# Performance work log

Hardware: AMD Instinct MI355X
Metric: run time of the kernel (lower is better)

The kernel has to match this reference:

```python
import jax, jax.numpy as jnp
import numpy as np

B, H, W, C = 32, 56, 56, 512
WS, SHIFT, NH = 7, 3, 16
N = WS * WS
NW = (H // WS) * (W // WS)
HID = 4 * C
EPS = 1e-5


def _np_constants():
    # log-spaced relative coords table (SwinV2 CPB input), pretrained_window_size=[0,0]
    rh = np.arange(-(WS - 1), WS, dtype=np.float32)
    tbl = np.stack(np.meshgrid(rh, rh, indexing='ij'), axis=-1)  # (2*WS-1, 2*WS-1, 2)
    tbl = tbl / (WS - 1) * 8.0
    tbl = np.sign(tbl) * np.log2(np.abs(tbl) + 1.0) / np.log2(8.0)
    coords = np.stack(np.meshgrid(np.arange(WS), np.arange(WS), indexing='ij'))
    cf = coords.reshape(2, -1)
    rc = (cf[:, :, None] - cf[:, None, :]).transpose(1, 2, 0).copy()  # (N,N,2)
    rc[..., 0] += WS - 1
    rc[..., 1] += WS - 1
    rc[..., 0] *= 2 * WS - 1
    rpi = rc.sum(-1)  # (N,N) indices into the (2*WS-1)^2 table
    # shifted-window attention mask
    img = np.zeros((H, W), dtype=np.float32)
    sl = (slice(0, -WS), slice(-WS, -SHIFT), slice(-SHIFT, None))
    cnt = 0
    for hs in sl:
        for ws in sl:
            img[hs, ws] = cnt
            cnt += 1
    mw = img.reshape(H // WS, WS, W // WS, WS).transpose(0, 2, 1, 3).reshape(-1, N)
    am = mw[:, None, :] - mw[:, :, None]
    attn_mask = np.where(am != 0, -100.0, 0.0).astype(np.float32)  # (NW,N,N)
    return tbl.reshape(-1, 2).astype(np.float32), rpi.reshape(-1), attn_mask

TBL_NP, RPI_NP, MASK_NP = _np_constants()


def _ln(x, g, b):
    mu = jnp.mean(x, -1, keepdims=True)
    var = jnp.mean((x - mu) ** 2, -1, keepdims=True)
    return (x - mu) * jax.lax.rsqrt(var + EPS) * g + b


def _win_part(x):  # (B,H,W,C) -> (B*NW, N, C)
    x = x.reshape(B, H // WS, WS, W // WS, WS, C).transpose(0, 1, 3, 2, 4, 5)
    return x.reshape(-1, N, C)


def _win_rev(w):  # (B*NW, N, C) -> (B,H,W,C)
    x = w.reshape(B, H // WS, W // WS, WS, WS, C).transpose(0, 1, 3, 2, 4, 5)
    return x.reshape(B, H, W, C)


def setup_inputs() -> dict:
    key = jax.random.key(0)
    ks = jax.random.split(key, 8)
    s = 0.02
    return {
        'x': jax.random.normal(ks[0], (B, H * W, C), jnp.float32),
        'qkv_w': jax.random.normal(ks[1], (3 * C, C), jnp.float32) * s,
        'q_bias': jnp.zeros((C,), jnp.float32),
        'v_bias': jnp.zeros((C,), jnp.float32),
        'logit_scale': jnp.log(10.0) * jnp.ones((NH, 1, 1), jnp.float32),
        'cpb_w1': jax.random.normal(ks[2], (512, 2), jnp.float32) * s,
        'cpb_b1': jnp.zeros((512,), jnp.float32),
        'cpb_w2': jax.random.normal(ks[3], (NH, 512), jnp.float32) * s,
        'proj_w': jax.random.normal(ks[4], (C, C), jnp.float32) * s,
        'proj_b': jnp.zeros((C,), jnp.float32),
        'norm1_g': jnp.ones((C,), jnp.float32),
        'norm1_b': jnp.zeros((C,), jnp.float32),
        'fc1_w': jax.random.normal(ks[5], (HID, C), jnp.float32) * s,
        'fc1_b': jnp.zeros((HID,), jnp.float32),
        'fc2_w': jax.random.normal(ks[6], (C, HID), jnp.float32) * s,
        'fc2_b': jnp.zeros((C,), jnp.float32),
        'norm2_g': jnp.ones((C,), jnp.float32),
        'norm2_b': jnp.zeros((C,), jnp.float32),
    }


def reference(x, qkv_w, q_bias, v_bias, logit_scale, cpb_w1, cpb_b1, cpb_w2,
              proj_w, proj_b, norm1_g, norm1_b, fc1_w, fc1_b, fc2_w, fc2_b,
              norm2_g, norm2_b):
    tbl = jnp.asarray(TBL_NP)
    mask = jnp.asarray(MASK_NP)
    shortcut = x
    xi = x.reshape(B, H, W, C)
    xi = jnp.roll(xi, shift=(-SHIFT, -SHIFT), axis=(1, 2))
    xw = _win_part(xi)  # (B*NW, N, C)
    qkv_bias = jnp.concatenate([q_bias, jnp.zeros_like(v_bias), v_bias])
    qkv = xw @ qkv_w.T + qkv_bias
    qkv = qkv.reshape(-1, N, 3, NH, C // NH).transpose(2, 0, 3, 1, 4)
    q, k, v = qkv[0], qkv[1], qkv[2]  # (B_, NH, N, hd)
    qn = q / jnp.maximum(jnp.linalg.norm(q, axis=-1, keepdims=True), 1e-12)
    kn = k / jnp.maximum(jnp.linalg.norm(k, axis=-1, keepdims=True), 1e-12)
    scale = jnp.exp(jnp.minimum(logit_scale, jnp.log(100.0)))  # (NH,1,1)
    attn = jnp.einsum('bhnd,bhmd->bhnm', qn, kn) * scale
    # CPB MLP -> relative position bias
    hcb = jax.nn.relu(tbl @ cpb_w1.T + cpb_b1)       # (169, 512)
    bias_tbl = hcb @ cpb_w2.T                        # (169, NH)
    rpb = bias_tbl[RPI_NP].reshape(N, N, NH).transpose(2, 0, 1)
    rpb = 16.0 * jax.nn.sigmoid(rpb)
    attn = attn + rpb[None]
    attn = attn.reshape(B, NW, NH, N, N) + mask[None, :, None]
    attn = jax.nn.softmax(attn.reshape(-1, NH, N, N), axis=-1)
    out = jnp.einsum('bhnm,bhmd->bhnd', attn, v).transpose(0, 2, 1, 3).reshape(-1, N, C)
    out = out @ proj_w.T + proj_b
    xi = _win_rev(out)
    xi = jnp.roll(xi, shift=(SHIFT, SHIFT), axis=(1, 2)).reshape(B, H * W, C)
    x = shortcut + _ln(xi, norm1_g, norm1_b)  # SwinV2 post-norm residual
    hmlp = jax.nn.gelu(x @ fc1_w.T + fc1_b, approximate=False)
    m = hmlp @ fc2_w.T + fc2_b
    x = x + _ln(m, norm2_g, norm2_b)
    return x
```

## Files before the change

### kernel.cpp

```cpp
#include <hip/hip_runtime.h>

typedef unsigned short u16;
typedef unsigned int   u32;

using f32x4  = __attribute__((ext_vector_type(4))) float;
using bf16x8 = __attribute__((ext_vector_type(8))) short;

__device__ __forceinline__ float bf2f(u16 u){
  union { u32 i; float f; } x; x.i = ((u32)u) << 16; return x.f;
}
__device__ __forceinline__ u16 f2bf(float f){
  union { float f; u32 i; } x; x.f = f;
  u32 r = x.i + 0x7FFFu + ((x.i >> 16) & 1u);
  return (u16)(r >> 16);
}
__device__ __forceinline__ float gelu_f(float v){
  float u = 0.7978845608f * v * (1.f + 0.044715f*v*v);
  float e = __expf(2.f*u);
  return 0.5f*v*(2.f - 2.f/(e + 1.f));
}

__device__ __forceinline__ void glds16(const void* g, void* l){
  __builtin_amdgcn_global_load_lds(
      (const __attribute__((address_space(1))) unsigned int*)g,
      (__attribute__((address_space(3))) unsigned int*)(unsigned int)(unsigned long long)l,
      16, 0, 0);
}

__device__ __forceinline__ int rollmap(int m){
  int win = m / 49, n = m % 49;
  int b  = win >> 6, wi = win & 63;
  int wh = wi >> 3, ww = wi & 7;
  int r = n / 7, c = n % 7;
  int sh = wh*7 + r + 3; if (sh >= 56) sh -= 56;
  int sw = ww*7 + c + 3; if (sw >= 56) sw -= 56;
  return b*3136 + sh*56 + sw;
}

template<int EPI, int AMODE, int NT>
__global__ __launch_bounds__(256) void gemm_bt(const u16* __restrict__ A,
      const u16* __restrict__ Bw, const float* __restrict__ bias,
      void* __restrict__ outp, int M, int N, int nbn)
{
  constexpr int K = NT * 32;
  __shared__ __align__(16) char LDS[3*16384];
  const int t    = threadIdx.x;
  const int lane = t & 63, wave = t >> 6;
  const int wm = wave >> 1, wn = wave & 1;

  const int gl = ((blockIdx.x & 7) * ((int)gridDim.x >> 3)) + (blockIdx.x >> 3);
  const int bm = gl / nbn, bn = gl - bm*nbn;

  const int r0 = t >> 2;
  const int sc = t & 3;
  const int dc = sc ^ ((r0 >> 1) & 3);

  const u16* gB0 = Bw + (size_t)(bn*128 + r0)*K + dc*8;
  const u16* gB1 = gB0 + (size_t)64*K;
  const u16* gA0; const u16* gA1;
  if constexpr (AMODE == 0){
    gA0 = A + (size_t)(bm*128 + r0)*K + dc*8;
    gA1 = gA0 + (size_t)64*K;
  } else {
    gA0 = A + (size_t)rollmap(bm*128 + r0     )*K + dc*8;
    gA1 = A + (size_t)rollmap(bm*128 + r0 + 64)*K + dc*8;
  }

  const int lr = lane & 15, lk = lane >> 4;
  int offA[4], offB[4];
#pragma unroll
  for (int i = 0; i < 4; ++i){
    int ar = wm*64 + i*16 + lr;
    offA[i] = ar*64 + ((lk ^ ((ar >> 1) & 3)) * 16);
    int br = wn*64 + i*16 + lr;
    offB[i] = br*64 + ((lk ^ ((br >> 1) & 3)) * 16);
  }

  f32x4 acc[4][4];
#pragma unroll
  for (int i = 0; i < 4; ++i)
#pragma unroll
    for (int j = 0; j < 4; ++j) acc[i][j] = (f32x4){0.f, 0.f, 0.f, 0.f};

  auto STAGE = [&](int kt, int buf){
    char* Ld = LDS + buf*16384;
    glds16(gA0 + kt, Ld +         wave*1024);
    glds16(gA1 + kt, Ld +  4096 + wave*1024);
    glds16(gB0 + kt, Ld +  8192 + wave*1024);
    glds16(gB1 + kt, Ld + 12288 + wave*1024);
  };
  auto COMPUTE = [&](int buf){
    const char* Ld = LDS + buf*16384;
    bf16x8 fa[4], fb[4];
#pragma unroll
    for (int i = 0; i < 4; ++i){
      fa[i] = *(const bf16x8*)(Ld + offA[i]);
      fb[i] = *(const bf16x8*)(Ld + 8192 + offB[i]);
    }
#pragma unroll
    for (int i = 0; i < 4; ++i)
#pragma unroll
      for (int j = 0; j < 4; ++j)
        acc[i][j] = __builtin_amdgcn_mfma_f32_16x16x32_bf16(fa[i], fb[j], acc[i][j], 0, 0, 0);
  };

  STAGE(0, 0);
  STAGE(32, 1);
  asm volatile("s_waitcnt vmcnt(4)" ::: "memory");
  __builtin_amdgcn_s_barrier();
  asm volatile("" ::: "memory");

  if constexpr (NT <= 24){
#pragma unroll
    for (int t2 = 0; t2 < NT; ++t2){
      if (t2 + 2 < NT) STAGE((t2 + 2) * 32, (t2 + 2) % 3);
      COMPUTE(t2 % 3);
      if (t2 + 2 < NT){
        asm volatile("s_waitcnt vmcnt(4) lgkmcnt(0)" ::: "memory");
      } else if (t2 + 1 < NT){
        asm volatile("s_waitcnt vmcnt(0) lgkmcnt(0)" ::: "memory");
      }
      if (t2 + 1 < NT){
        __builtin_amdgcn_s_barrier();
        asm volatile("" ::: "memory");
      }
    }
  } else {
    int cur = 0;
    for (int t2 = 0; t2 + 2 < NT; ++t2){
      int nx2 = cur + 2; if (nx2 >= 3) nx2 -= 3;
      STAGE((t2 + 2) * 32, nx2);
      COMPUTE(cur);
      asm volatile("s_waitcnt vmcnt(4) lgkmcnt(0)" ::: "memory");
      __builtin_amdgcn_s_barrier();
      asm volatile("" ::: "memory");
      ++cur; if (cur == 3) cur = 0;
    }
    COMPUTE(cur);
    asm volatile("s_waitcnt vmcnt(0) lgkmcnt(0)" ::: "memory");
    __builtin_amdgcn_s_barrier();
    asm volatile("" ::: "memory");
    ++cur; if (cur == 3) cur = 0;
    COMPUTE(cur);
  }

#pragma unroll
  for (int i = 0; i < 4; ++i){
#pragma unroll
    for (int j = 0; j < 4; ++j){
      int cm = bm*128 + wm*64 + i*16 + (lane >> 4)*4;
      int cn = bn*128 + wn*64 + j*16 + (lane & 15);
      float bv = bias[cn];
#pragma unroll
      for (int r = 0; r < 4; ++r){
        float v = acc[i][j][r] + bv;
        if (EPI == 2) v = gelu_f(v);
        if (EPI == 1) ((float*)outp)[(size_t)(cm + r)*N + cn] = v;
        else          ((u16*)  outp)[(size_t)(cm + r)*N + cn] = f2bf(v);
      }
    }
  }
}

__global__ __launch_bounds__(256, 2) void attn_mfma(const u16* __restrict__ qkv,
      const float* __restrict__ rpb, const float* __restrict__ ls,
      u16* __restrict__ outp)
{
  __shared__ __align__(16) u16 Pl[4][64*72];
  __shared__ __align__(16) u16 Vl[4][32*72];
  __shared__ unsigned char regid[64];
  const int tid  = threadIdx.x, lane = tid & 63, wave = tid >> 6;
  const int lc = lane & 15, lg = lane >> 4;
  const int pair = blockIdx.x*4 + wave;
  const int win = pair >> 4, h = pair & 15;

  const u16* qb = qkv + (size_t)win*49*1536 + h*32;
  const u16* kb = qb + 512;
  const u16* vb = qb + 1024;

  if (tid < 49){
    int wi = win & 63, wh = wi >> 3, ww = wi & 7;
    int q7 = (tid*37) >> 8, r7 = tid - q7*7;
    int gh = wh*7 + q7, gw = ww*7 + r7;
    int rh = gh < 49 ? 0 : (gh < 53 ? 1 : 2);
    int rw = gw < 49 ? 0 : (gw < 53 ? 1 : 2);
    regid[tid] = (unsigned char)(rh*3 + rw);
  }

  u16* V = &Vl[wave][0];
#pragma unroll
  for (int it = 0; it < 4; ++it){
    int ch = it*64 + lane;
    int n = ch >> 2, oct = ch & 3;
    union { int4 i4; u16 s[8]; } v8;
    if (n < 49) v8.i4 = *(const int4*)(vb + (size_t)n*1536 + oct*8);
    else        v8.i4 = make_int4(0,0,0,0);
#pragma unroll
    for (int q = 0; q < 8; ++q) V[(oct*8 + q)*72 + n] = v8.s[q];
  }

  const float scale = __expf(fminf(ls[h], 4.6051702f));
  bf16x8 qf[4], kf[4];
#pragma unroll
  for (int ti = 0; ti < 4; ++ti){
    const int n = ti*16 + lc;
    {
      union { int4 i4; u16 s[8]; } raw;
      raw.i4 = *(const int4*)(qb + (size_t)n*1536 + lg*8);
      float f[8]; float ss = 0.f;
#pragma unroll
      for (int q = 0; q < 8; ++q){ f[q] = bf2f(raw.s[q]); ss += f[q]*f[q]; }
      ss += __shfl_xor(ss, 16); ss += __shfl_xor(ss, 32);
      const float inv = scale / fmaxf(sqrtf(ss), 1e-12f);
      union { short s[8]; bf16x8 v; } o;
#pragma unroll
      for (int q = 0; q < 8; ++q) o.s[q] = (short)f2bf(f[q]*inv);
      qf[ti] = o.v;
    }
    {
      union { int4 i4; u16 s[8]; } raw;
      raw.i4 = *(const int4*)(kb + (size_t)n*1536 + lg*8);
      float f[8]; float ss = 0.f;
#pragma unroll
      for (int q = 0; q < 8; ++q){ f[q] = bf2f(raw.s[q]); ss += f[q]*f[q]; }
      ss += __shfl_xor(ss, 16); ss += __shfl_xor(ss, 32);
      const float inv = 1.f / fmaxf(sqrtf(ss), 1e-12f);
      union { short s[8]; bf16x8 v; } o;
#pragma unroll
      for (int q = 0; q < 8; ++q) o.s[q] = (short)f2bf(f[q]*inv);
      kf[ti] = o.v;
    }
  }
  __syncthreads();

  f32x4 acc[4][4];
#pragma unroll
  for (int i = 0; i < 4; ++i)
#pragma unroll
    for (int j = 0; j < 4; ++j) acc[i][j] = (f32x4){0.f,0.f,0.f,0.f};
#pragma unroll
  for (int i = 0; i < 4; ++i)
#pragma unroll
    for (int j = 0; j < 4; ++j)
      acc[i][j] = __builtin_amdgcn_mfma_f32_16x16x32_bf16(qf[i], kf[j], acc[i][j], 0, 0, 0);

  u16* P = &Pl[wave][0];
  int rj[4];
#pragma unroll
  for (int tj = 0; tj < 4; ++tj){
    int j = tj*16 + lc;
    rj[tj] = (int)regid[j < 49 ? j : 0];
  }
  const float* rpbh = rpb + h*2401;
#pragma unroll
  for (int ti = 0; ti < 4; ++ti){
#pragma unroll
    for (int r = 0; r < 4; ++r){
      const int i = ti*16 + lg*4 + r;
      const bool iv = i < 49;
      const int ic = iv ? i : 0;
      const int ri = (int)regid[ic];
      const float* rrow = rpbh + ic*49;
      float sv[4];
#pragma unroll
      for (int tj = 0; tj < 4; ++tj){
        const int j = tj*16 + lc;
        float t2 = acc[ti][tj][r] + rrow[j < 49 ? j : 0];
        if (ri != rj[tj]) t2 -= 100.f;
        sv[tj] = (iv && j < 49) ? t2 : -1e30f;
      }
      float mx = fmaxf(fmaxf(sv[0],sv[1]), fmaxf(sv[2],sv[3]));
      mx = fmaxf(mx, __shfl_xor(mx, 1));
      mx = fmaxf(mx, __shfl_xor(mx, 2));
      mx = fmaxf(mx, __shfl_xor(mx, 4));
      mx = fmaxf(mx, __shfl_xor(mx, 8));
      float p[4], sum = 0.f;
#pragma unroll
      for (int tj = 0; tj < 4; ++tj){ p[tj] = __expf(sv[tj] - mx); sum += p[tj]; }
      sum += __shfl_xor(sum, 1); sum += __shfl_xor(sum, 2);
      sum += __shfl_xor(sum, 4); sum += __shfl_xor(sum, 8);
      const float rs = __builtin_amdgcn_rcpf(sum);
#pragma unroll
      for (int tj = 0; tj < 4; ++tj) P[i*72 + tj*16 + lc] = f2bf(p[tj]*rs);
    }
  }
  __syncthreads();

  f32x4 o[4][2];
#pragma unroll
  for (int i = 0; i < 4; ++i){ o[i][0] = (f32x4){0.f,0.f,0.f,0.f}; o[i][1] = (f32x4){0.f,0.f,0.f,0.f}; }
#pragma unroll
  for (int ks = 0; ks < 2; ++ks){
    bf16x8 pa[4], vf[2];
#pragma unroll
    for (int ti = 0; ti < 4; ++ti)
      pa[ti] = *(const bf16x8*)((const char*)P + (ti*16 + lc)*144 + (ks*4 + lg)*16);
#pragma unroll
    for (int tc = 0; tc < 2; ++tc)
      vf[tc] = *(const bf16x8*)((const char*)V + (tc*16 + lc)*144 + (ks*4 + lg)*16);
#pragma unroll
    for (int ti = 0; ti < 4; ++ti)
#pragma unroll
      for (int tc = 0; tc < 2; ++tc)
        o[ti][tc] = __builtin_amdgcn_mfma_f32_16x16x32_bf16(pa[ti], vf[tc], o[ti][tc], 0, 0, 0);
  }

#pragma unroll
  for (int ti = 0; ti < 4; ++ti){
#pragma unroll
    for (int tc = 0; tc < 2; ++tc){
#pragma unroll
      for (int r = 0; r < 4; ++r){
        const int i = ti*16 + lg*4 + r;
        if (i < 49)
          outp[((size_t)win*49 + i)*512 + h*32 + tc*16 + lc] = f2bf(o[ti][tc][r]);
      }
    }
  }
}

__global__ __launch_bounds__(256) void ln1_kernel(const u16* __restrict__ xb,
      const u16* __restrict__ y, const float* __restrict__ g, const float* __restrict__ bt,
      float* __restrict__ xout, u16* __restrict__ xbf)
{
  __shared__ float red[8];
  const int t = blockIdx.x;
  const int b = t / 3136, s = t % 3136;
  const int hh = s / 56, ww2 = s % 56;
  int ph = hh + 53; if (ph >= 56) ph -= 56;
  int pw = ww2 + 53; if (pw >= 56) pw -= 56;
  const int win = b*64 + (ph/7)*8 + (pw/7);
  const int n   = (ph%7)*7 + (pw%7);
  const u16* yr = y + ((size_t)win*49 + n)*512;
  const int c = threadIdx.x * 2;
  u32 u = *(const u32*)(yr + c);
  float vx = bf2f((u16)(u & 0xffff)), vy = bf2f((u16)(u >> 16));
  float sum = vx + vy, sq = vx*vx + vy*vy;
#pragma unroll
  for (int off = 32; off; off >>= 1){ sum += __shfl_xor(sum, off); sq += __shfl_xor(sq, off); }
  if ((threadIdx.x & 63) == 0){ red[threadIdx.x >> 6] = sum; red[(threadIdx.x >> 6) + 4] = sq; }
  __syncthreads();
  sum = red[0]+red[1]+red[2]+red[3];
  sq  = red[4]+red[5]+red[6]+red[7];
  const float mu  = sum * (1.f/512.f);
  const float inv = rsqrtf(fmaxf(sq * (1.f/512.f) - mu*mu, 0.f) + 1e-5f);
  u32 ux = *(const u32*)(xb + (size_t)t*512 + c);
  float o0 = bf2f((u16)(ux & 0xffff)) + (vx - mu)*inv*g[c]   + bt[c];
  float o1 = bf2f((u16)(ux >> 16))    + (vy - mu)*inv*g[c+1] + bt[c+1];
  float* orow = xout + (size_t)t*512;
  orow[c] = o0; orow[c+1] = o1;
  *(u32*)(xbf + (size_t)t*512 + c) = (u32)f2bf(o0) | ((u32)f2bf(o1) << 16);
}

__global__ __launch_bounds__(256) void ln2_kernel(const u16* __restrict__ m,
      const float* __restrict__ g, const float* __restrict__ bt, float* __restrict__ out)
{
  __shared__ float red[8];
  const int t = blockIdx.x;
  const int c = threadIdx.x * 2;
  u32 u = *(const u32*)(m + (size_t)t*512 + c);
  float v0 = bf2f((u16)(u & 0xffff)), v1 = bf2f((u16)(u >> 16));
  float sum = v0 + v1, sq = v0*v0 + v1*v1;
#pragma unroll
  for (int off = 32; off; off >>= 1){ sum += __shfl_xor(sum, off); sq += __shfl_xor(sq, off); }
  if ((threadIdx.x & 63) == 0){ red[threadIdx.x >> 6] = sum; red[(threadIdx.x >> 6) + 4] = sq; }
  __syncthreads();
  sum = red[0]+red[1]+red[2]+red[3];
  sq  = red[4]+red[5]+red[6]+red[7];
  const float mu  = sum * (1.f/512.f);
  const float inv = rsqrtf(fmaxf(sq * (1.f/512.f) - mu*mu, 0.f) + 1e-5f);
  float* orow = out + (size_t)t*512;
  orow[c]   += (v0 - mu)*inv*g[c]   + bt[c];
  orow[c+1] += (v1 - mu)*inv*g[c+1] + bt[c+1];
}

__global__ void cast_bf16_kernel(const float* __restrict__ in, u16* __restrict__ out, int n4){
  int i = blockIdx.x*256 + threadIdx.x;
  if (i >= n4) return;
  float4 v = *(const float4*)(in + (size_t)i*4);
  u32 lo = (u32)f2bf(v.x) | ((u32)f2bf(v.y) << 16);
  u32 hi = (u32)f2bf(v.z) | ((u32)f2bf(v.w) << 16);
  *(uint2*)(out + (size_t)i*4) = make_uint2(lo, hi);
}
__global__ void qkvbias_kernel(const float* __restrict__ qb, const float* __restrict__ vb,
                               float* __restrict__ out){
  int i = blockIdx.x*256 + threadIdx.x;
  if (i >= 1536) return;
  out[i] = i < 512 ? qb[i] : (i < 1024 ? 0.f : vb[i - 1024]);
}
__device__ __forceinline__ float cpb_coord(int d){
  float v = (float)(d - 6) * (8.f/6.f);
  float m = log2f(fabsf(v) + 1.f) * (1.f/3.f);
  return v > 0.f ? m : (v < 0.f ? -m : 0.f);
}
__global__ void cpb_kernel(const float* __restrict__ w1, const float* __restrict__ b1,
                           const float* __restrict__ w2, float* __restrict__ btbl){
  int idx = blockIdx.x*256 + threadIdx.x;
  if (idx >= 169*16) return;
  int e = idx >> 4, h = idx & 15;
  float t0 = cpb_coord(e / 13), t1 = cpb_coord(e % 13);
  float acc = 0.f;
  for (int jj = 0; jj < 512; ++jj){
    float hid = fmaxf(t0*w1[jj*2] + t1*w1[jj*2+1] + b1[jj], 0.f);
    acc += hid * w2[h*512 + jj];
  }
  btbl[e*16 + h] = acc;
}
__global__ void rpb_kernel(const float* __restrict__ btbl, float* __restrict__ rpb){
  int idx = blockIdx.x*256 + threadIdx.x;
  if (idx >= 16*49*49) return;
  int hh = idx / 2401, ij = idx % 2401, i = ij / 49, j = ij % 49;
  int dr = i/7 - j/7 + 6, dc = i%7 - j%7 + 6;
  float bb = btbl[(dr*13 + dc)*16 + hh];
  rpb[idx] = 16.f / (1.f + __expf(-bb));
}

extern "C" void kernel_launch(void* const* d_in, const int* in_sizes, int n_in,
                              void* d_out, int out_size, void* d_ws, size_t ws_size,
                              hipStream_t stream)
{
  const float* x    = (const float*)d_in[0];
  const float* qkvw = (const float*)d_in[1];
  const float* qb   = (const float*)d_in[2];
  const float* vb   = (const float*)d_in[3];
  const float* ls   = (const float*)d_in[4];
  const float* cw1  = (const float*)d_in[5];
  const float* cb1  = (const float*)d_in[6];
  const float* cw2  = (const float*)d_in[7];
  const float* pw   = (const float*)d_in[8];
  const float* pb   = (const float*)d_in[9];
  const float* n1g  = (const float*)d_in[10];
  const float* n1b  = (const float*)d_in[11];
  const float* f1w  = (const float*)d_in[12];
  const float* f1b  = (const float*)d_in[13];
  const float* f2w  = (const float*)d_in[14];
  const float* f2b  = (const float*)d_in[15];
  const float* n2g  = (const float*)d_in[16];
  const float* n2b  = (const float*)d_in[17];

  char* ws = (char*)d_ws;
  const size_t SZ_BIG = (size_t)100352 * 2048 * 2;
  const size_t SZ_MID = (size_t)100352 * 512  * 2;
  size_t o = SZ_BIG + SZ_MID;
  u16* wqkv  = (u16*)(ws + o); o += (size_t)1536*512*2;
  u16* wproj = (u16*)(ws + o); o += (size_t)512*512*2;
  u16* wfc1  = (u16*)(ws + o); o += (size_t)2048*512*2;
  u16* wfc2  = (u16*)(ws + o); o += (size_t)512*2048*2;
  float* qkvbias = (float*)(ws + o); o += 1536*4;
  float* btbl    = (float*)(ws + o); o += 2704*4;
  float* rpb     = (float*)(ws + o); o += 38416*4;

  u16*   xbf   = (u16*)ws;
  u16*   qkvo  = (u16*)(ws + (size_t)100352*512*2);
  u16*   y_h   = qkvo;
  u16*   big_h = (u16*)ws;
  u16*   mid   = (u16*)(ws + SZ_BIG);
  float* out   = (float*)d_out;

  cast_bf16_kernel<<<768,  256, 0, stream>>>(qkvw, wqkv, 1536*512/4);
  cast_bf16_kernel<<<256,  256, 0, stream>>>(pw,  wproj, 512*512/4);
  cast_bf16_kernel<<<1024, 256, 0, stream>>>(f1w, wfc1, 2048*512/4);
  cast_bf16_kernel<<<1024, 256, 0, stream>>>(f2w, wfc2, 512*2048/4);
  qkvbias_kernel<<<6, 256, 0, stream>>>(qb, vb, qkvbias);
  cpb_kernel<<<11, 256, 0, stream>>>(cw1, cb1, cw2, btbl);
  rpb_kernel<<<151, 256, 0, stream>>>(btbl, rpb);
  cast_bf16_kernel<<<50176, 256, 0, stream>>>(x, xbf, 100352*512/4);

  gemm_bt<0,2,16><<<784*12, 256, 0, stream>>>(xbf, wqkv, qkvbias,
                                              (void*)qkvo, 100352, 1536, 12);
  attn_mfma<<<8192, 256, 0, stream>>>(qkvo, rpb, ls, mid);
  gemm_bt<0,0,16><<<784*4, 256, 0, stream>>>(mid, wproj, pb,
                                             (void*)y_h, 100352, 512, 4);
  ln1_kernel<<<100352, 256, 0, stream>>>(xbf, y_h, n1g, n1b, out, mid);
  gemm_bt<2,0,16><<<784*16, 256, 0, stream>>>(mid, wfc1, f1b,
                                              (void*)big_h, 100352, 2048, 16);
  gemm_bt<0,0,64><<<784*4, 256, 0, stream>>>(big_h, wfc2, f2b,
                                             (void*)mid, 100352, 512, 4);
  ln2_kernel<<<100352, 256, 0, stream>>>(mid, n2g, n2b, out);
}
```

Baseline: 1.559 ms.

## Rewrite GEMM as 256x256 tile, 8-wave kernel with ping-pong staged loads

Replaces the 128x128, 4-wave GEMM with a 256x256 tile, 8-wave kernel. It uses 64-wide K steps, two 64KB LDS buffers and a new XOR swizzle. Loads for the next tiles are interleaved between four MFMA sub-phases, with barriers and s_setprio raising MFMA priority. The goal is more data reuse per byte loaded and better overlap of global-to-LDS traffic with compute for all four dense GEMMs. In exchange it uses 128KB of LDS per block, more accumulator registers and many more barriers, which could limit occupancy.

```diff
diff --git a/kernel.cpp b/kernel.cpp
--- a/kernel.cpp
+++ b/kernel.cpp
@@ -37,126 +37,169 @@
   return b*3136 + sh*56 + sw;
 }
 
-template<int EPI, int AMODE, int NT>
-__global__ __launch_bounds__(256) void gemm_bt(const u16* __restrict__ A,
+template<int EPI, int AMODE, int NKT>
+__global__ __launch_bounds__(512, 2) void gemm_bt(const u16* __restrict__ A,
       const u16* __restrict__ Bw, const float* __restrict__ bias,
       void* __restrict__ outp, int M, int N, int nbn)
 {
-  constexpr int K = NT * 32;
-  __shared__ __align__(16) char LDS[3*16384];
+  constexpr int K = NKT * 64;
+  __shared__ __align__(16) char LDS[2*65536];
   const int t    = threadIdx.x;
   const int lane = t & 63, wave = t >> 6;
-  const int wm = wave >> 1, wn = wave & 1;
+  const int wr = wave >> 2, wn = wave & 3;
+  const int lr = lane & 15, lk = lane >> 4;
 
   const int gl = ((blockIdx.x & 7) * ((int)gridDim.x >> 3)) + (blockIdx.x >> 3);
   const int bm = gl / nbn, bn = gl - bm*nbn;
 
-  const int r0 = t >> 2;
-  const int sc = t & 3;
-  const int dc = sc ^ ((r0 >> 1) & 3);
-
-  const u16* gB0 = Bw + (size_t)(bn*128 + r0)*K + dc*8;
-  const u16* gB1 = gB0 + (size_t)64*K;
-  const u16* gA0; const u16* gA1;
+  const int q   = (t & 7) ^ ((t >> 3) & 7);
+  const int sr0 = 2*(t >> 3) + (q >> 2);
+  const int sch = (q & 3) * 8;
+  const u16 *pA0, *pA1;
   if constexpr (AMODE == 0){
-    gA0 = A + (size_t)(bm*128 + r0)*K + dc*8;
-    gA1 = gA0 + (size_t)64*K;
+    pA0 = A + (size_t)(bm*256 + sr0      )*K + sch;
+    pA1 = A + (size_t)(bm*256 + sr0 + 128)*K + sch;
   } else {
-    gA0 = A + (size_t)rollmap(bm*128 + r0     )*K + dc*8;
-    gA1 = A + (size_t)rollmap(bm*128 + r0 + 64)*K + dc*8;
-  }
-
-  const int lr = lane & 15, lk = lane >> 4;
-  int offA[4], offB[4];
-#pragma unroll
-  for (int i = 0; i < 4; ++i){
-    int ar = wm*64 + i*16 + lr;
-    offA[i] = ar*64 + ((lk ^ ((ar >> 1) & 3)) * 16);
-    int br = wn*64 + i*16 + lr;
-    offB[i] = br*64 + ((lk ^ ((br >> 1) & 3)) * 16);
-  }
-
-  f32x4 acc[4][4];
-#pragma unroll
-  for (int i = 0; i < 4; ++i)
+    pA0 = A + (size_t)rollmap(bm*256 + sr0      )*K + sch;
+    pA1 = A + (size_t)rollmap(bm*256 + sr0 + 128)*K + sch;
+  }
+  const u16* pB0 = Bw + (size_t)(bn*256 + sr0      )*K + sch;
+  const u16* pB1 = Bw + (size_t)(bn*256 + sr0 + 128)*K + sch;
+
+  int oA[8], oB[4];
+#pragma unroll
+  for (int i = 0; i < 8; ++i){
+    int r = wr*128 + i*16 + lr;
+    oA[i] = ((r>>1)<<7) + (((((r&1)<<2)|lk) ^ ((r>>1)&7))<<4);
+  }
+#pragma unroll
+  for (int j = 0; j < 4; ++j){
+    int r = wn*64 + j*16 + lr;
+    oB[j] = ((r>>1)<<7) + (((((r&1)<<2)|lk) ^ ((r>>1)&7))<<4);
+  }
+
+  f32x4 acc[8][4];
+#pragma unroll
+  for (int i = 0; i < 8; ++i)
 #pragma unroll
     for (int j = 0; j < 4; ++j) acc[i][j] = (f32x4){0.f, 0.f, 0.f, 0.f};
 
-  auto STAGE = [&](int kt, int buf){
-    char* Ld = LDS + buf*16384;
-    glds16(gA0 + kt, Ld +         wave*1024);
-    glds16(gA1 + kt, Ld +  4096 + wave*1024);
-    glds16(gB0 + kt, Ld +  8192 + wave*1024);
-    glds16(gB1 + kt, Ld + 12288 + wave*1024);
+  auto stgA = [&](int T, int ks, int buf){
+    char* d = LDS + buf*65536 + ks*16384 + wave*1024;
+    const int e = T*64 + ks*32;
+    glds16(pA0 + e, d);
+    glds16(pA1 + e, d + 8192);
   };
-  auto COMPUTE = [&](int buf){
-    const char* Ld = LDS + buf*16384;
+  auto stgB = [&](int T, int ks, int buf){
+    char* d = LDS + buf*65536 + 32768 + ks*16384 + wave*1024;
+    const int e = T*64 + ks*32;
+    glds16(pB0 + e, d);
+    glds16(pB1 + e, d + 8192);
+  };
+
+  stgA(0,0,0); stgA(0,1,0); stgB(0,0,0); stgB(0,1,0);
+  stgA(1,0,1); stgA(1,1,1); stgB(1,0,1); stgB(1,1,1);
+  asm volatile("s_waitcnt vmcnt(8)" ::: "memory");
+  __builtin_amdgcn_s_barrier();
+  asm volatile("" ::: "memory");
+
+  auto TILE = [&](int T, int buf){
+    const char* ld = LDS + buf*65536;
+    const bool stP0  = (T >= 1) && (T+1 < NKT);
+    const bool st123 = (T+2 < NKT);
     bf16x8 fa[4], fb[4];
-#pragma unroll
-    for (int i = 0; i < 4; ++i){
-      fa[i] = *(const bf16x8*)(Ld + offA[i]);
-      fb[i] = *(const bf16x8*)(Ld + 8192 + offB[i]);
-    }
+
+#pragma unroll
+    for (int j = 0; j < 4; ++j) fb[j] = *(const bf16x8*)(ld + 32768 + oB[j]);
+#pragma unroll
+    for (int i = 0; i < 4; ++i) fa[i] = *(const bf16x8*)(ld + oA[i]);
+    if (stP0) stgA(T+1, 1, buf^1);
+    __builtin_amdgcn_s_barrier();
+    asm volatile("s_waitcnt lgkmcnt(0)" ::: "memory");
+    __builtin_amdgcn_sched_barrier(0);
+    __builtin_amdgcn_s_setprio(1);
 #pragma unroll
     for (int i = 0; i < 4; ++i)
 #pragma unroll
       for (int j = 0; j < 4; ++j)
         acc[i][j] = __builtin_amdgcn_mfma_f32_16x16x32_bf16(fa[i], fb[j], acc[i][j], 0, 0, 0);
-  };
-
-  STAGE(0, 0);
-  STAGE(32, 1);
-  asm volatile("s_waitcnt vmcnt(4)" ::: "memory");
-  __builtin_amdgcn_s_barrier();
-  asm volatile("" ::: "memory");
-
-  if constexpr (NT <= 24){
-#pragma unroll
-    for (int t2 = 0; t2 < NT; ++t2){
-      if (t2 + 2 < NT) STAGE((t2 + 2) * 32, (t2 + 2) % 3);
-      COMPUTE(t2 % 3);
-      if (t2 + 2 < NT){
-        asm volatile("s_waitcnt vmcnt(4) lgkmcnt(0)" ::: "memory");
-      } else if (t2 + 1 < NT){
-        asm volatile("s_waitcnt vmcnt(0) lgkmcnt(0)" ::: "memory");
-      }
-      if (t2 + 1 < NT){
-        __builtin_amdgcn_s_barrier();
-        asm volatile("" ::: "memory");
-      }
-    }
-  } else {
-    int cur = 0;
-    for (int t2 = 0; t2 + 2 < NT; ++t2){
-      int nx2 = cur + 2; if (nx2 >= 3) nx2 -= 3;
-      STAGE((t2 + 2) * 32, nx2);
-      COMPUTE(cur);
-      asm volatile("s_waitcnt vmcnt(4) lgkmcnt(0)" ::: "memory");
+    __builtin_amdgcn_s_setprio(0);
+    __builtin_amdgcn_s_barrier();
+    asm volatile("" ::: "memory");
+
+#pragma unroll
+    for (int i = 0; i < 4; ++i) fa[i] = *(const bf16x8*)(ld + oA[4+i]);
+    if (st123) stgB(T+2, 0, buf);
+    __builtin_amdgcn_s_barrier();
+    asm volatile("s_waitcnt lgkmcnt(0)" ::: "memory");
+    __builtin_amdgcn_sched_barrier(0);
+    __builtin_amdgcn_s_setprio(1);
+#pragma unroll
+    for (int i = 0; i < 4; ++i)
+#pragma unroll
+      for (int j = 0; j < 4; ++j)
+        acc[4+i][j] = __builtin_amdgcn_mfma_f32_16x16x32_bf16(fa[i], fb[j], acc[4+i][j], 0, 0, 0);
+    __builtin_amdgcn_s_setprio(0);
+    __builtin_amdgcn_s_barrier();
+    asm volatile("" ::: "memory");
+
+#pragma unroll
+    for (int j = 0; j < 4; ++j) fb[j] = *(const bf16x8*)(ld + 49152 + oB[j]);
+#pragma unroll
+    for (int i = 0; i < 4; ++i) fa[i] = *(const bf16x8*)(ld + 16384 + oA[i]);
+    if (st123) stgA(T+2, 0, buf);
+    __builtin_amdgcn_s_barrier();
+    asm volatile("s_waitcnt lgkmcnt(0)" ::: "memory");
+    __builtin_amdgcn_sched_barrier(0);
+    __builtin_amdgcn_s_setprio(1);
+#pragma unroll
+    for (int i = 0; i < 4; ++i)
+#pragma unroll
+      for (int j = 0; j < 4; ++j)
+        acc[i][j] = __builtin_amdgcn_mfma_f32_16x16x32_bf16(fa[i], fb[j], acc[i][j], 0, 0, 0);
+    __builtin_amdgcn_s_setprio(0);
+    __builtin_amdgcn_s_barrier();
+    asm volatile("" ::: "memory");
+
+#pragma unroll
+    for (int i = 0; i < 4; ++i) fa[i] = *(const bf16x8*)(ld + 16384 + oA[4+i]);
+    if (st123) stgB(T+2, 1, buf);
+    __builtin_amdgcn_s_barrier();
+    asm volatile("s_waitcnt lgkmcnt(0)" ::: "memory");
+    __builtin_amdgcn_sched_barrier(0);
+    __builtin_amdgcn_s_setprio(1);
+#pragma unroll
+    for (int i = 0; i < 4; ++i)
+#pragma unroll
+      for (int j = 0; j < 4; ++j)
+        acc[4+i][j] = __builtin_amdgcn_mfma_f32_16x16x32_bf16(fa[i], fb[j], acc[4+i][j], 0, 0, 0);
+    __builtin_amdgcn_s_setprio(0);
+    if (T <= NKT-3)      asm volatile("s_waitcnt vmcnt(6)" ::: "memory");
+    else if (T == NKT-2) asm volatile("s_waitcnt vmcnt(0)" ::: "memory");
+    if (T < NKT-1){
       __builtin_amdgcn_s_barrier();
       asm volatile("" ::: "memory");
-      ++cur; if (cur == 3) cur = 0;
     }
-    COMPUTE(cur);
-    asm volatile("s_waitcnt vmcnt(0) lgkmcnt(0)" ::: "memory");
-    __builtin_amdgcn_s_barrier();
-    asm volatile("" ::: "memory");
-    ++cur; if (cur == 3) cur = 0;
-    COMPUTE(cur);
-  }
-
-#pragma unroll
-  for (int i = 0; i < 4; ++i){
+  };
+
+  for (int p = 0; p < NKT/2; ++p){
+    TILE(2*p,     0);
+    TILE(2*p + 1, 1);
+  }
+
+  const int lc = lane & 15, lg = lane >> 4;
+#pragma unroll
+  for (int i = 0; i < 8; ++i){
 #pragma unroll
     for (int j = 0; j < 4; ++j){
-      int cm = bm*128 + wm*64 + i*16 + (lane >> 4)*4;
-      int cn = bn*128 + wn*64 + j*16 + (lane & 15);
+      int cm = bm*256 + wr*128 + i*16 + lg*4;
+      int cn = bn*256 + wn*64  + j*16 + lc;
       float bv = bias[cn];
 #pragma unroll
       for (int r = 0; r < 4; ++r){
         float v = acc[i][j][r] + bv;
         if (EPI == 2) v = gelu_f(v);
-        if (EPI == 1) ((float*)outp)[(size_t)(cm + r)*N + cn] = v;
-        else          ((u16*)  outp)[(size_t)(cm + r)*N + cn] = f2bf(v);
+        ((u16*)outp)[(size_t)(cm + r)*N + cn] = f2bf(v);
       }
     }
   }
@@ -466,15 +509,15 @@
   rpb_kernel<<<151, 256, 0, stream>>>(btbl, rpb);
   cast_bf16_kernel<<<50176, 256, 0, stream>>>(x, xbf, 100352*512/4);
 
-  gemm_bt<0,2,16><<<784*12, 256, 0, stream>>>(xbf, wqkv, qkvbias,
-                                              (void*)qkvo, 100352, 1536, 12);
+  gemm_bt<0,2,8><<<392*6, 512, 0, stream>>>(xbf, wqkv, qkvbias,
+                                            (void*)qkvo, 100352, 1536, 6);
   attn_mfma<<<8192, 256, 0, stream>>>(qkvo, rpb, ls, mid);
-  gemm_bt<0,0,16><<<784*4, 256, 0, stream>>>(mid, wproj, pb,
-                                             (void*)y_h, 100352, 512, 4);
+  gemm_bt<0,0,8><<<392*2, 512, 0, stream>>>(mid, wproj, pb,
+                                            (void*)y_h, 100352, 512, 2);
   ln1_kernel<<<100352, 256, 0, stream>>>(xbf, y_h, n1g, n1b, out, mid);
-  gemm_bt<2,0,16><<<784*16, 256, 0, stream>>>(mid, wfc1, f1b,
-                                              (void*)big_h, 100352, 2048, 16);
-  gemm_bt<0,0,64><<<784*4, 256, 0, stream>>>(big_h, wfc2, f2b,
-                                             (void*)mid, 100352, 512, 4);
+  gemm_bt<2,0,8><<<392*8, 512, 0, stream>>>(mid, wfc1, f1b,
+                                            (void*)big_h, 100352, 2048, 8);
+  gemm_bt<0,0,32><<<392*2, 512, 0, stream>>>(big_h, wfc2, f2b,
+                                             (void*)mid, 100352, 512, 2);
   ln2_kernel<<<100352, 256, 0, stream>>>(mid, n2g, n2b, out);
 }
```

Measured after the change: 1.454 ms. -6.7%, faster.
